# Optimization experiments

Measured on AMD Instinct MI355X. Metric: run time of the kernel, lower is better.

## Reference

```python
import jax, jax.numpy as jnp
import numpy as np

N = 50000      # nodes
E = 800000     # edges
IN = 128       # in_channels
H = 128        # hidden_channels
L = 3          # num_layers
CONF_H = 64    # confidence_hidden_dim
TAU0 = 1.0


def _linear_params(key, fan_in, fan_out, bias=True):
    k1, k2 = jax.random.split(key)
    lim = 1.0 / np.sqrt(fan_in)
    w = jax.random.uniform(k1, (fan_in, fan_out), jnp.float32, -lim, lim)
    if bias:
        b = jax.random.uniform(k2, (fan_out,), jnp.float32, -lim, lim)
        return w, b
    return w


def setup_inputs() -> dict:
    key = jax.random.key(0)
    ks = jax.random.split(key, 20)
    x = jax.random.normal(ks[0], (N, IN), jnp.float32)
    edge_index = jax.random.randint(ks[1], (2, E), 0, N, jnp.int32)
    gnoise_soft = jax.random.gumbel(ks[2], (L, N, 2), jnp.float32)
    gnoise_hard = jax.random.gumbel(ks[3], (L, N, 2), jnp.float32)
    conv_w0, conv_b0 = _linear_params(ks[4], IN, H)
    conv_w1, conv_b1 = _linear_params(ks[5], H, H)
    conv_w2, conv_b2 = _linear_params(ks[6], H, H)
    soft_w1, soft_b1 = _linear_params(ks[7], H, CONF_H)
    soft_w2, soft_b2 = _linear_params(ks[8], CONF_H, 2)
    hard_w1, hard_b1 = _linear_params(ks[9], H + 1, CONF_H)
    hard_w2, hard_b2 = _linear_params(ks[10], CONF_H, 2)
    temp_w = _linear_params(ks[11], H, 1, bias=False)
    return dict(x=x, edge_index=edge_index, gnoise_soft=gnoise_soft, gnoise_hard=gnoise_hard,
                conv_w0=conv_w0, conv_b0=conv_b0, conv_w1=conv_w1, conv_b1=conv_b1,
                conv_w2=conv_w2, conv_b2=conv_b2,
                soft_w1=soft_w1, soft_b1=soft_b1, soft_w2=soft_w2, soft_b2=soft_b2,
                hard_w1=hard_w1, hard_b1=hard_b1, hard_w2=hard_w2, hard_b2=hard_b2,
                temp_w=temp_w)


def _forward(x, edge_index, gnoise_soft, gnoise_hard,
             conv_w0, conv_b0, conv_w1, conv_b1, conv_w2, conv_b2,
             soft_w1, soft_b1, soft_w2, soft_b2,
             hard_w1, hard_b1, hard_w2, hard_b2, temp_w):
    src, dst = edge_index[0], edge_index[1]
    loop = jnp.arange(N, dtype=src.dtype)
    # GCN symmetric normalization with self-loops (PyG gcn_norm)
    src_sl = jnp.concatenate([src, loop])
    dst_sl = jnp.concatenate([dst, loop])
    deg = jax.ops.segment_sum(jnp.ones(E + N, x.dtype), dst_sl, num_segments=N)
    dinv = jnp.where(deg > 0, jax.lax.rsqrt(deg), 0.0)
    norm = dinv[src_sl] * dinv[dst_sl]  # [E+N]
    # readiness graph: self-loops removed
    nonself = (src != dst).astype(x.dtype)
    deg_ns = jnp.clip(jax.ops.segment_sum(nonself, src, num_segments=N), 1.0)

    conv_params = [(conv_w0, conv_b0), (conv_w1, conv_b1), (conv_w2, conv_b2)]
    z = jnp.zeros((N, H), x.dtype)
    soft_exited = jnp.zeros(N, bool)
    hard_exited = jnp.zeros(N, bool)
    exit_layers = jnp.full((N,), L, jnp.int32)
    active = []
    h = x
    for li in range(L):
        W, b = conv_params[li]
        hw = h @ W  # [N,H]
        h = jax.ops.segment_sum(norm[:, None] * hw[src_sl], dst_sl, num_segments=N) + b
        if li < L - 1:
            h = jax.nn.gelu(h, approximate=False)  # torch F.gelu default (dropout p=0)
        active.append(jnp.sum(~hard_exited).astype(jnp.int32))
        # temperature head: 1 / (softplus(Wx) + tau0)
        temp = 1.0 / (jax.nn.softplus(h @ temp_w) + TAU0)  # [N,1]
        temp = jnp.where(jnp.isinf(temp), 0.0, temp)
        # soft exit head + gumbel softmax (hard=False)
        soft_logits = jax.nn.relu(h @ soft_w1 + soft_b1) @ soft_w2 + soft_b2  # [N,2]
        sg = jax.nn.softmax((soft_logits + gnoise_soft[li]) / temp, axis=-1)
        soft_dec = sg[:, 1] > sg[:, 0]
        soft_exited = soft_exited | (soft_dec & ~soft_exited)
        # neighbor readiness: mean of soft_exited over non-self neighbors (detached)
        ready_sum = jax.ops.segment_sum(soft_exited[dst].astype(x.dtype) * nonself, src, num_segments=N)
        readiness = jax.lax.stop_gradient((ready_sum / deg_ns)[:, None])
        hin = jnp.concatenate([h, readiness], axis=-1)  # [N,H+1]
        hard_logits = jax.nn.relu(hin @ hard_w1 + hard_b1) @ hard_w2 + hard_b2
        cont = jnp.concatenate([jnp.full((N, 1), 1e6, x.dtype), jnp.zeros((N, 1), x.dtype)], axis=-1)
        eff = jnp.where(soft_exited[:, None], hard_logits, cont)
        hg = jax.nn.softmax((eff + gnoise_hard[li]) / temp, axis=-1)
        hard_dec = hg[:, 1] > hg[:, 0]
        newly = hard_dec & ~hard_exited
        z = z + h * newly[:, None].astype(x.dtype)
        exit_layers = jnp.where(newly, jnp.int32(li), exit_layers)
        hard_exited = hard_exited | newly
    z = z + h * (~hard_exited)[:, None].astype(x.dtype)
    return z, exit_layers, jnp.stack(active)


def reference(x, edge_index, gnoise_soft, gnoise_hard,
              conv_w0, conv_b0, conv_w1, conv_b1, conv_w2, conv_b2,
              soft_w1, soft_b1, soft_w2, soft_b2,
              hard_w1, hard_b1, hard_w2, hard_b2, temp_w):
    return _forward(x, edge_index, gnoise_soft, gnoise_hard,
                    conv_w0, conv_b0, conv_w1, conv_b1, conv_w2, conv_b2,
                    soft_w1, soft_b1, soft_w2, soft_b2,
                    hard_w1, hard_b1, hard_w2, hard_b2, temp_w)
```

## Files before the change

### kernel.cpp

```cpp
#include <hip/hip_runtime.h>
#include <hip/hip_bf16.h>
#include <math.h>

#define NN 50000
#define EE 800000
#define HH 128
#define CHH 64
#define LL 3
#define ZT (NN * HH)
#define NBK 196
#define EPB 3125

using bf16 = __hip_bfloat16;
typedef unsigned short u16;
typedef unsigned int u32;
typedef __attribute__((ext_vector_type(8))) short s16x8;
typedef __attribute__((ext_vector_type(4))) float f32x4;

__device__ __forceinline__ float ldbf(const u16* p, size_t i) {
    return __uint_as_float(((u32)p[i]) << 16);
}
__device__ __forceinline__ u16 f2b(float v) {
    bf16 b = __float2bfloat16(v);
    return *reinterpret_cast<u16*>(&b);
}
__device__ __forceinline__ void stbf(u16* p, size_t i, float v) { p[i] = f2b(v); }
__device__ __forceinline__ float blo(u32 w) { return __uint_as_float(w << 16); }
__device__ __forceinline__ float bhi(u32 w) { return __uint_as_float(w & 0xFFFF0000u); }

__global__ __launch_bounds__(256) void zero_out_k(float* __restrict__ out, int n) {
    int i = blockIdx.x * 256 + threadIdx.x;
    if (i < n) out[i] = 0.f;
}

__global__ __launch_bounds__(256) void init_k(const float* __restrict__ x, u16* __restrict__ h,
        int* __restrict__ softex, int* __restrict__ hardex, int* __restrict__ exitl,
        int* __restrict__ act) {
    int i = blockIdx.x * 256 + threadIdx.x;
    if (i < ZT) stbf(h, (size_t)i, x[i]);
    if (i < NN) { softex[i] = 0; hardex[i] = 0; exitl[i] = LL; }
    if (i < LL) act[i] = 0;
}

__global__ __launch_bounds__(256) void hist_k(const int* __restrict__ ei, int keyoff, int skipself,
        int* __restrict__ hist) {
    __shared__ int hh[NBK];
    int t = threadIdx.x, b = blockIdx.x;
    if (t < NBK) hh[t] = 0;
    __syncthreads();
    int base = b * EPB;
    for (int i = t; i < EPB; i += 256) {
        int e = base + i;
        int s = ei[e], d = ei[EE + e];
        if ((u32)s >= NN || (u32)d >= NN) continue;
        if (skipself && s == d) continue;
        int key = keyoff ? d : s;
        atomicAdd(&hh[key >> 8], 1);
    }
    __syncthreads();
    if (t < NBK) hist[b * NBK + t] = hh[t];
}

__global__ __launch_bounds__(256) void boffs_k(const int* __restrict__ hist,
        int* __restrict__ boffs, int* __restrict__ bstart) {
    int t = threadIdx.x;
    __shared__ int scn[256];
    int run = 0;
    if (t < NBK) {
        for (int b = 0; b < 256; ++b) {
            boffs[t * 256 + b] = run;
            run += hist[b * NBK + t];
        }
    }
    int v = (t < NBK) ? run : 0;
    scn[t] = v;
    __syncthreads();
    for (int off = 1; off < 256; off <<= 1) {
        int x = (t >= off) ? scn[t - off] : 0;
        __syncthreads();
        scn[t] += x;
        __syncthreads();
    }
    int excl = scn[t] - v;
    if (t < NBK) {
        bstart[t] = excl;
        if (t == NBK - 1) bstart[NBK] = excl + v;
        for (int b = 0; b < 256; ++b) boffs[t * 256 + b] += excl;
    }
}

__global__ __launch_bounds__(256) void scat_k(const int* __restrict__ ei, int keyoff, int skipself,
        const int* __restrict__ boffs, u32* __restrict__ ebuf) {
    __shared__ int cur[NBK];
    int t = threadIdx.x, b = blockIdx.x;
    if (t < NBK) cur[t] = boffs[t * 256 + b];
    __syncthreads();
    int base = b * EPB;
    for (int i = t; i < EPB; i += 256) {
        int e = base + i;
        int s = ei[e], d = ei[EE + e];
        if ((u32)s >= NN || (u32)d >= NN) continue;
        if (skipself && s == d) continue;
        int key = keyoff ? d : s;
        int other = keyoff ? s : d;
        int pos = atomicAdd(&cur[key >> 8], 1);
        ebuf[pos] = (u32)other | ((u32)(key & 255) << 16);
    }
}

__global__ __launch_bounds__(256) void fine_k(const u32* __restrict__ ebuf,
        const int* __restrict__ bstart, int* __restrict__ rowptr, u16* __restrict__ csrx,
        float* __restrict__ dinv, int addself) {
    __shared__ int cnt[256];
    __shared__ int scn[256];
    int t = threadIdx.x, bk = blockIdx.x;
    int eb = bstart[bk], ee = bstart[bk + 1];
    cnt[t] = 0;
    __syncthreads();
    for (int i = eb + t; i < ee; i += 256)
        atomicAdd(&cnt[(ebuf[i] >> 16) & 255], 1);
    __syncthreads();
    int v = cnt[t];
    scn[t] = v;
    __syncthreads();
    for (int off = 1; off < 256; off <<= 1) {
        int x = (t >= off) ? scn[t - off] : 0;
        __syncthreads();
        scn[t] += x;
        __syncthreads();
    }
    int excl = scn[t] - v;
    int n = (bk << 8) + t;
    if (n < NN) {
        rowptr[n] = eb + excl;
        if (dinv) dinv[n] = 1.0f / sqrtf((float)(v + addself));
    }
    if (bk == NBK - 1 && t == 0) rowptr[NN] = ee;
    cnt[t] = excl;
    __syncthreads();
    for (int i = eb + t; i < ee; i += 256) {
        u32 w = ebuf[i];
        int lo = (w >> 16) & 255;
        int pos = atomicAdd(&cnt[lo], 1);
        csrx[eb + pos] = (u16)(w & 0xFFFF);
    }
}

__global__ __launch_bounds__(256) void pack_w_k(const float* __restrict__ w0,
        const float* __restrict__ w1, const float* __restrict__ w2,
        const float* __restrict__ sw1, const float* __restrict__ hw1, u16* __restrict__ wt) {
    int i = blockIdx.x * 256 + threadIdx.x;
    if (i >= 4 * HH * HH) return;
    int mat = i >> 14, rr = i & 16383, o = rr >> 7, k = rr & 127;
    float v;
    if (mat == 0) v = w0[k * HH + o];
    else if (mat == 1) v = w1[k * HH + o];
    else if (mat == 2) v = w2[k * HH + o];
    else v = (o < CHH) ? sw1[k * CHH + o] : hw1[k * CHH + (o - CHH)];
    stbf(wt, (size_t)i, v);
}

__global__ __launch_bounds__(256) void gather_hin_k(const int* __restrict__ rowptr,
        const u16* __restrict__ csrc, const float* __restrict__ dinv,
        const u16* __restrict__ h, u16* __restrict__ hinb) {
    int node = blockIdx.x * 4 + (threadIdx.x >> 6);
    int lane = threadIdx.x & 63;
    int beg = rowptr[node], end = rowptr[node + 1];
    float dvd = dinv[node];
    float a0 = 0.f, a1 = 0.f;
    int e = beg;
    for (; e + 3 < end; e += 4) {
        int s0 = csrc[e], s1 = csrc[e + 1], s2 = csrc[e + 2], s3 = csrc[e + 3];
        float n0 = dinv[s0], n1 = dinv[s1], n2 = dinv[s2], n3 = dinv[s3];
        u32 w0 = *(const u32*)(h + (size_t)s0 * HH + lane * 2);
        u32 w1 = *(const u32*)(h + (size_t)s1 * HH + lane * 2);
        u32 w2 = *(const u32*)(h + (size_t)s2 * HH + lane * 2);
        u32 w3 = *(const u32*)(h + (size_t)s3 * HH + lane * 2);
        a0 = fmaf(n0, blo(w0), a0); a1 = fmaf(n0, bhi(w0), a1);
        a0 = fmaf(n1, blo(w1), a0); a1 = fmaf(n1, bhi(w1), a1);
        a0 = fmaf(n2, blo(w2), a0); a1 = fmaf(n2, bhi(w2), a1);
        a0 = fmaf(n3, blo(w3), a0); a1 = fmaf(n3, bhi(w3), a1);
    }
    for (; e < end; ++e) {
        int s0 = csrc[e];
        float n0 = dinv[s0];
        u32 w0 = *(const u32*)(h + (size_t)s0 * HH + lane * 2);
        a0 = fmaf(n0, blo(w0), a0); a1 = fmaf(n0, bhi(w0), a1);
    }
    a0 *= dvd; a1 *= dvd;
    u32 hw = *(const u32*)(h + (size_t)node * HH + lane * 2);
    float self = dvd * dvd;
    a0 = fmaf(blo(hw), self, a0);
    a1 = fmaf(bhi(hw), self, a1);
    u32 pk = (u32)f2b(a0) | ((u32)f2b(a1) << 16);
    ((u32*)hinb)[(size_t)node * 64 + lane] = pk;
}

__global__ __launch_bounds__(256) void fused_gemm_k(int li, u16* __restrict__ hinb,
        const u16* __restrict__ Wc, const u16* __restrict__ Wh,
        const float* __restrict__ bias, int geluf, u16* __restrict__ h,
        const float* __restrict__ sb1, const float* __restrict__ sw2, const float* __restrict__ sb2,
        const float* __restrict__ gs, int* __restrict__ softex) {
    __shared__ u16 hl[16 * HH];
    __shared__ float l0s[2][16], l1s[2][16];
    int wave = threadIdx.x >> 6, lane = threadIdx.x & 63;
    int row0 = blockIdx.x * 16;
    int r = lane & 15, g = lane >> 4;
    const u16* arow = hinb + (size_t)(row0 + r) * HH;
    s16x8 af[4];
    #pragma unroll
    for (int kk = 0; kk < 4; ++kk) af[kk] = *(const s16x8*)(arow + kk * 32 + g * 8);
    f32x4 acc[2];
    #pragma unroll
    for (int cc = 0; cc < 2; ++cc) {
        int c0 = wave * 32 + cc * 16;
        const u16* brow = Wc + (size_t)(c0 + r) * HH;
        f32x4 a = {0.f, 0.f, 0.f, 0.f};
        #pragma unroll
        for (int kk = 0; kk < 4; ++kk) {
            s16x8 b = *(const s16x8*)(brow + kk * 32 + g * 8);
            a = __builtin_amdgcn_mfma_f32_16x16x32_bf16(af[kk], b, a, 0, 0, 0);
        }
        acc[cc] = a;
    }
    #pragma unroll
    for (int cc = 0; cc < 2; ++cc) {
        int col = wave * 32 + cc * 16 + r;
        float bv = bias[col];
        #pragma unroll
        for (int j = 0; j < 4; ++j) {
            int row = g * 4 + j;
            float v = acc[cc][j] + bv;
            if (geluf) v = 0.5f * v * (1.0f + erff(v * 0.70710678118654752f));
            stbf(h, (size_t)(row0 + row) * HH + col, v);
            int chunk = (col >> 3) ^ (row & 7);
            hl[row * HH + chunk * 8 + (col & 7)] = f2b(v);
        }
    }
    __syncthreads();
    #pragma unroll
    for (int kk = 0; kk < 4; ++kk) {
        int k0 = kk * 32 + g * 8;
        int chunk = (k0 >> 3) ^ (r & 7);
        af[kk] = *(const s16x8*)(hl + r * HH + chunk * 8);
    }
    #pragma unroll
    for (int cc = 0; cc < 2; ++cc) {
        int c0 = wave * 32 + cc * 16;
        const u16* brow = Wh + (size_t)(c0 + r) * HH;
        f32x4 a = {0.f, 0.f, 0.f, 0.f};
        #pragma unroll
        for (int kk = 0; kk < 4; ++kk) {
            s16x8 b = *(const s16x8*)(brow + kk * 32 + g * 8);
            a = __builtin_amdgcn_mfma_f32_16x16x32_bf16(af[kk], b, a, 0, 0, 0);
        }
        acc[cc] = a;
    }
    if (wave < 2) {
        float pl0[4] = {0.f, 0.f, 0.f, 0.f}, pl1[4] = {0.f, 0.f, 0.f, 0.f};
        #pragma unroll
        for (int cc = 0; cc < 2; ++cc) {
            int col = wave * 32 + cc * 16 + r;
            float b1 = sb1[col], w20 = sw2[col * 2], w21 = sw2[col * 2 + 1];
            #pragma unroll
            for (int j = 0; j < 4; ++j) {
                float hv = fmaxf(acc[cc][j] + b1, 0.f);
                pl0[j] = fmaf(hv, w20, pl0[j]);
                pl1[j] = fmaf(hv, w21, pl1[j]);
            }
        }
        #pragma unroll
        for (int off = 1; off < 16; off <<= 1) {
            #pragma unroll
            for (int j = 0; j < 4; ++j) {
                pl0[j] += __shfl_xor(pl0[j], off);
                pl1[j] += __shfl_xor(pl1[j], off);
            }
        }
        if (r == 0) {
            #pragma unroll
            for (int j = 0; j < 4; ++j) {
                l0s[wave][g * 4 + j] = pl0[j];
                l1s[wave][g * 4 + j] = pl1[j];
            }
        }
    } else {
        #pragma unroll
        for (int cc = 0; cc < 2; ++cc) {
            int col = wave * 32 + cc * 16 + r;
            #pragma unroll
            for (int j = 0; j < 4; ++j) {
                int row = g * 4 + j;
                stbf(hinb, (size_t)(row0 + row) * HH + col, acc[cc][j]);
            }
        }
    }
    __syncthreads();
    if (threadIdx.x < 16) {
        int row = threadIdx.x, n = row0 + row;
        float l0 = l0s[0][row] + l0s[1][row] + sb2[0];
        float l1 = l1s[0][row] + l1s[1][row] + sb2[1];
        const float* gg = gs + ((size_t)li * NN + n) * 2;
        if (l1 + gg[1] > l0 + gg[0]) softex[n] = 1;
    }
}

__global__ __launch_bounds__(256) void hard_fin_k(int li, const u16* __restrict__ P,
        const u16* __restrict__ h, const float* __restrict__ hw1, const float* __restrict__ hb1,
        const float* __restrict__ hw2, const float* __restrict__ hb2,
        const float* __restrict__ gh, const int* __restrict__ softex,
        int* __restrict__ hardex, int* __restrict__ exitl,
        const int* __restrict__ orow, const u16* __restrict__ ocol,
        float* __restrict__ out) {
    int t = threadIdx.x;
    int n = blockIdx.x * 4 + (t >> 6);
    int j = t & 63;
    if (!softex[n] || hardex[n]) return;
    int ob = orow[n], oe = orow[n + 1];
    int cnt = 0;
    for (int e = ob + j; e < oe; e += 64) cnt += softex[ocol[e]];
    #pragma unroll
    for (int off = 32; off > 0; off >>= 1) cnt += __shfl_xor(cnt, off);
    int dns = oe - ob; if (dns < 1) dns = 1;
    float r = (float)cnt / (float)dns;
    float pv = ldbf(P, (size_t)n * HH + CHH + j);
    float hid = fmaxf(pv + r * hw1[HH * CHH + j] + hb1[j], 0.f);
    float l0 = hid * hw2[j * 2], l1 = hid * hw2[j * 2 + 1];
    #pragma unroll
    for (int off = 32; off > 0; off >>= 1) {
        l0 += __shfl_xor(l0, off);
        l1 += __shfl_xor(l1, off);
    }
    const float* g = gh + ((size_t)li * NN + n) * 2;
    if (l1 + hb2[1] + g[1] > l0 + hb2[0] + g[0]) {
        if (j == 0) { hardex[n] = 1; exitl[n] = li; }
        u32 hw = *(const u32*)(h + (size_t)n * HH + j * 2);
        out[(size_t)n * HH + j * 2]     = blo(hw);
        out[(size_t)n * HH + j * 2 + 1] = bhi(hw);
    }
}

__global__ __launch_bounds__(256) void tail_k(const u16* __restrict__ h, const int* __restrict__ exitl,
        float* __restrict__ out, int* __restrict__ act) {
    __shared__ int c[LL];
    int t = threadIdx.x;
    int i = blockIdx.x * 256 + t;
    if (t < LL) c[t] = 0;
    __syncthreads();
    if (i < ZT) {
        int n = i >> 7;
        if (exitl[n] == LL) out[i] = ldbf(h, (size_t)i);
    } else if (i < ZT + NN) {
        int e = exitl[i - ZT];
        out[i] = (float)e;
        if (e < LL) atomicAdd(&c[e], 1);
    }
    __syncthreads();
    if (t < LL && c[t]) atomicAdd(&act[t], c[t]);
}

__global__ __launch_bounds__(64) void finalize_k(const int* __restrict__ act, float* __restrict__ out) {
    if (threadIdx.x == 0) {
        out[ZT + NN]     = (float)NN;
        out[ZT + NN + 1] = (float)(NN - act[0]);
        out[ZT + NN + 2] = (float)(NN - act[0] - act[1]);
    }
}

extern "C" void kernel_launch(void* const* d_in, const int* in_sizes, int n_in,
                              void* d_out, int out_size, void* d_ws, size_t ws_size,
                              hipStream_t stream) {
    float* out = (float*)d_out;
    const int OUT_N = ZT + NN + LL;

    static const int CANON[19] = {6400000,1600000,300000,300000,16384,128,16384,128,16384,128,
                                  8192,64,128,2,8256,64,128,2,128};
    static const int SORTED_ROLE[19] = {5,7,9,4,6,8,1,3,2,15,17,14,16,11,13,10,12,18,0};
    int perm[19];
    bool ok = (n_in == 19);
    if (ok) {
        bool mc = true, mr = true, ms = true;
        for (int i = 0; i < 19; ++i) {
            if (in_sizes[i] != CANON[i]) mc = false;
            if (in_sizes[i] != CANON[18 - i]) mr = false;
            if (in_sizes[i] != CANON[SORTED_ROLE[i]]) ms = false;
        }
        if (mc)      for (int c = 0; c < 19; ++c) perm[c] = c;
        else if (mr) for (int c = 0; c < 19; ++c) perm[c] = 18 - c;
        else if (ms) { for (int p = 0; p < 19; ++p) perm[SORTED_ROLE[p]] = p; }
        else         for (int c = 0; c < 19; ++c) perm[c] = c;
    }
    if (!ok) {
        zero_out_k<<<(OUT_N + 255) / 256, 256, 0, stream>>>(out, OUT_N);
        return;
    }

    const float* x  = (const float*)d_in[perm[0]];
    const int*   ei = (const int*)d_in[perm[1]];
    const float* gs = (const float*)d_in[perm[2]];
    const float* gh = (const float*)d_in[perm[3]];
    const float* cw[3] = { (const float*)d_in[perm[4]], (const float*)d_in[perm[6]], (const float*)d_in[perm[8]] };
    const float* cb[3] = { (const float*)d_in[perm[5]], (const float*)d_in[perm[7]], (const float*)d_in[perm[9]] };
    const float* sw1 = (const float*)d_in[perm[10]];
    const float* sb1 = (const float*)d_in[perm[11]];
    const float* sw2 = (const float*)d_in[perm[12]];
    const float* sb2 = (const float*)d_in[perm[13]];
    const float* hw1 = (const float*)d_in[perm[14]];
    const float* hb1 = (const float*)d_in[perm[15]];
    const float* hw2 = (const float*)d_in[perm[16]];
    const float* hb2 = (const float*)d_in[perm[17]];

    const size_t H_B    = (size_t)ZT * 2;
    const size_t FLAG_B = 200192;
    const size_t ACT_B  = 256;
    const size_t RP_B   = 200704;
    const size_t CE_B   = (size_t)EE * 2;
    const size_t WT_B   = 4 * HH * HH * 2;
    const size_t need = 2 * H_B + 4 * FLAG_B + ACT_B + 2 * RP_B + 2 * CE_B + WT_B;
    if (ws_size < need) {
        zero_out_k<<<(OUT_N + 255) / 256, 256, 0, stream>>>(out, OUT_N);
        return;
    }

    char* p = (char*)d_ws;
    u16* h    = (u16*)p; p += H_B;
    u16* hinb = (u16*)p; p += H_B;
    int* softex = (int*)p; p += FLAG_B;
    int* hardex = (int*)p; p += FLAG_B;
    int* exitl  = (int*)p; p += FLAG_B;
    float* dinv = (float*)p; p += FLAG_B;
    int* act    = (int*)p; p += ACT_B;
    int* irow   = (int*)p; p += RP_B;
    int* orow   = (int*)p; p += RP_B;
    u16* csrc   = (u16*)p; p += CE_B;
    u16* ocol   = (u16*)p; p += CE_B;
    u16* wt     = (u16*)p; p += WT_B;

    char* q = (char*)hinb;
    u32* ebuf  = (u32*)q;  q += (size_t)EE * 4;
    int* hist  = (int*)q;  q += 256 * NBK * 4;
    int* boffs = (int*)q;  q += NBK * 256 * 4;
    int* bstart = (int*)q; q += 1024;

    init_k<<<(ZT + 255) / 256, 256, 0, stream>>>(x, h, softex, hardex, exitl, act);

    hist_k<<<256, 256, 0, stream>>>(ei, 1, 0, hist);
    boffs_k<<<1, 256, 0, stream>>>(hist, boffs, bstart);
    scat_k<<<256, 256, 0, stream>>>(ei, 1, 0, boffs, ebuf);
    fine_k<<<NBK, 256, 0, stream>>>(ebuf, bstart, irow, csrc, dinv, 1);
    hist_k<<<256, 256, 0, stream>>>(ei, 0, 1, hist);
    boffs_k<<<1, 256, 0, stream>>>(hist, boffs, bstart);
    scat_k<<<256, 256, 0, stream>>>(ei, 0, 1, boffs, ebuf);
    fine_k<<<NBK, 256, 0, stream>>>(ebuf, bstart, orow, ocol, nullptr, 0);

    pack_w_k<<<(4 * HH * HH + 255) / 256, 256, 0, stream>>>(cw[0], cw[1], cw[2], sw1, hw1, wt);

    for (int li = 0; li < LL; ++li) {
        int geluf = (li < LL - 1) ? 1 : 0;
        gather_hin_k<<<NN / 4, 256, 0, stream>>>(irow, csrc, dinv, h, hinb);
        fused_gemm_k<<<NN / 16, 256, 0, stream>>>(li, hinb, wt + (size_t)li * HH * HH,
                                                  wt + (size_t)3 * HH * HH, cb[li], geluf, h,
                                                  sb1, sw2, sb2, gs, softex);
        hard_fin_k<<<NN / 4, 256, 0, stream>>>(li, hinb, h, hw1, hb1, hw2, hb2, gh, softex,
                                               hardex, exitl, orow, ocol, out);
    }
    tail_k<<<(OUT_N + 255) / 256, 256, 0, stream>>>(h, exitl, out, act);
    finalize_k<<<1, 64, 0, stream>>>(act, out);
}
```

Measured before the change: 415.4 us.

## Fuse neighbor gather into GEMM kernel and merge dual CSR builds

The per-layer neighbor aggregation is folded into the GEMM kernel: each block gathers its 16 rows straight into swizzled shared memory instead of writing and re-reading a bf16 hin buffer in global memory. The h buffers are ping-ponged between layers, and the hard-head projection partials are staged as fp32 in the output buffer for rows that have not exited. The two CSR builds (by destination and by source) are merged into single histogram, scatter and fine-sort launches, which cuts launches and reads of the edge list. The cost is less parallelism in the gather, since 4 rows per wave run serially inside a GEMM block, and extra workspace for the second edge buffer.

```diff
diff --git a/kernel.cpp b/kernel.cpp
--- a/kernel.cpp
+++ b/kernel.cpp
@@ -42,23 +42,22 @@
     if (i < LL) act[i] = 0;
 }
 
-__global__ __launch_bounds__(256) void hist_k(const int* __restrict__ ei, int keyoff, int skipself,
-        int* __restrict__ hist) {
-    __shared__ int hh[NBK];
+__global__ __launch_bounds__(256) void hist_both_k(const int* __restrict__ ei,
+        int* __restrict__ hist1, int* __restrict__ hist2) {
+    __shared__ int h1[NBK], h2[NBK];
     int t = threadIdx.x, b = blockIdx.x;
-    if (t < NBK) hh[t] = 0;
+    if (t < NBK) { h1[t] = 0; h2[t] = 0; }
     __syncthreads();
     int base = b * EPB;
     for (int i = t; i < EPB; i += 256) {
         int e = base + i;
         int s = ei[e], d = ei[EE + e];
         if ((u32)s >= NN || (u32)d >= NN) continue;
-        if (skipself && s == d) continue;
-        int key = keyoff ? d : s;
-        atomicAdd(&hh[key >> 8], 1);
-    }
-    __syncthreads();
-    if (t < NBK) hist[b * NBK + t] = hh[t];
+        atomicAdd(&h1[d >> 8], 1);
+        if (s != d) atomicAdd(&h2[s >> 8], 1);
+    }
+    __syncthreads();
+    if (t < NBK) { hist1[b * NBK + t] = h1[t]; hist2[b * NBK + t] = h2[t]; }
 }
 
 __global__ __launch_bounds__(256) void boffs_k(const int* __restrict__ hist,
@@ -89,31 +88,33 @@
     }
 }
 
-__global__ __launch_bounds__(256) void scat_k(const int* __restrict__ ei, int keyoff, int skipself,
-        const int* __restrict__ boffs, u32* __restrict__ ebuf) {
-    __shared__ int cur[NBK];
+__global__ __launch_bounds__(256) void scat_both_k(const int* __restrict__ ei,
+        const int* __restrict__ boffs1, u32* __restrict__ ebuf1,
+        const int* __restrict__ boffs2, u32* __restrict__ ebuf2) {
+    __shared__ int c1[NBK], c2[NBK];
     int t = threadIdx.x, b = blockIdx.x;
-    if (t < NBK) cur[t] = boffs[t * 256 + b];
+    if (t < NBK) { c1[t] = boffs1[t * 256 + b]; c2[t] = boffs2[t * 256 + b]; }
     __syncthreads();
     int base = b * EPB;
     for (int i = t; i < EPB; i += 256) {
         int e = base + i;
         int s = ei[e], d = ei[EE + e];
         if ((u32)s >= NN || (u32)d >= NN) continue;
-        if (skipself && s == d) continue;
-        int key = keyoff ? d : s;
-        int other = keyoff ? s : d;
-        int pos = atomicAdd(&cur[key >> 8], 1);
-        ebuf[pos] = (u32)other | ((u32)(key & 255) << 16);
-    }
-}
-
-__global__ __launch_bounds__(256) void fine_k(const u32* __restrict__ ebuf,
+        int pos = atomicAdd(&c1[d >> 8], 1);
+        ebuf1[pos] = (u32)s | ((u32)(d & 255) << 16);
+        if (s != d) {
+            int pos2 = atomicAdd(&c2[s >> 8], 1);
+            ebuf2[pos2] = (u32)d | ((u32)(s & 255) << 16);
+        }
+    }
+}
+
+__device__ __forceinline__ void fine_body(int bk, const u32* __restrict__ ebuf,
         const int* __restrict__ bstart, int* __restrict__ rowptr, u16* __restrict__ csrx,
         float* __restrict__ dinv, int addself) {
     __shared__ int cnt[256];
     __shared__ int scn[256];
-    int t = threadIdx.x, bk = blockIdx.x;
+    int t = threadIdx.x;
     int eb = bstart[bk], ee = bstart[bk + 1];
     cnt[t] = 0;
     __syncthreads();
@@ -136,6 +137,7 @@
         if (dinv) dinv[n] = 1.0f / sqrtf((float)(v + addself));
     }
     if (bk == NBK - 1 && t == 0) rowptr[NN] = ee;
+    __syncthreads();
     cnt[t] = excl;
     __syncthreads();
     for (int i = eb + t; i < ee; i += 256) {
@@ -144,6 +146,14 @@
         int pos = atomicAdd(&cnt[lo], 1);
         csrx[eb + pos] = (u16)(w & 0xFFFF);
     }
+}
+
+__global__ __launch_bounds__(256) void fine2_k(const u32* __restrict__ ebuf1,
+        const int* __restrict__ bstart1, int* __restrict__ irow, u16* __restrict__ csrc,
+        float* __restrict__ dinv, const u32* __restrict__ ebuf2,
+        const int* __restrict__ bstart2, int* __restrict__ orow, u16* __restrict__ ocol) {
+    if (blockIdx.x < NBK) fine_body(blockIdx.x, ebuf1, bstart1, irow, csrc, dinv, 1);
+    else                  fine_body(blockIdx.x - NBK, ebuf2, bstart2, orow, ocol, nullptr, 0);
 }
 
 __global__ __launch_bounds__(256) void pack_w_k(const float* __restrict__ w0,
@@ -160,56 +170,64 @@
     stbf(wt, (size_t)i, v);
 }
 
-__global__ __launch_bounds__(256) void gather_hin_k(const int* __restrict__ rowptr,
-        const u16* __restrict__ csrc, const float* __restrict__ dinv,
-        const u16* __restrict__ h, u16* __restrict__ hinb) {
-    int node = blockIdx.x * 4 + (threadIdx.x >> 6);
-    int lane = threadIdx.x & 63;
-    int beg = rowptr[node], end = rowptr[node + 1];
-    float dvd = dinv[node];
-    float a0 = 0.f, a1 = 0.f;
-    int e = beg;
-    for (; e + 3 < end; e += 4) {
-        int s0 = csrc[e], s1 = csrc[e + 1], s2 = csrc[e + 2], s3 = csrc[e + 3];
-        float n0 = dinv[s0], n1 = dinv[s1], n2 = dinv[s2], n3 = dinv[s3];
-        u32 w0 = *(const u32*)(h + (size_t)s0 * HH + lane * 2);
-        u32 w1 = *(const u32*)(h + (size_t)s1 * HH + lane * 2);
-        u32 w2 = *(const u32*)(h + (size_t)s2 * HH + lane * 2);
-        u32 w3 = *(const u32*)(h + (size_t)s3 * HH + lane * 2);
-        a0 = fmaf(n0, blo(w0), a0); a1 = fmaf(n0, bhi(w0), a1);
-        a0 = fmaf(n1, blo(w1), a0); a1 = fmaf(n1, bhi(w1), a1);
-        a0 = fmaf(n2, blo(w2), a0); a1 = fmaf(n2, bhi(w2), a1);
-        a0 = fmaf(n3, blo(w3), a0); a1 = fmaf(n3, bhi(w3), a1);
-    }
-    for (; e < end; ++e) {
-        int s0 = csrc[e];
-        float n0 = dinv[s0];
-        u32 w0 = *(const u32*)(h + (size_t)s0 * HH + lane * 2);
-        a0 = fmaf(n0, blo(w0), a0); a1 = fmaf(n0, bhi(w0), a1);
-    }
-    a0 *= dvd; a1 *= dvd;
-    u32 hw = *(const u32*)(h + (size_t)node * HH + lane * 2);
-    float self = dvd * dvd;
-    a0 = fmaf(blo(hw), self, a0);
-    a1 = fmaf(bhi(hw), self, a1);
-    u32 pk = (u32)f2b(a0) | ((u32)f2b(a1) << 16);
-    ((u32*)hinb)[(size_t)node * 64 + lane] = pk;
-}
-
-__global__ __launch_bounds__(256) void fused_gemm_k(int li, u16* __restrict__ hinb,
-        const u16* __restrict__ Wc, const u16* __restrict__ Wh,
-        const float* __restrict__ bias, int geluf, u16* __restrict__ h,
+__global__ __launch_bounds__(256) void mega_k(int li, int geluf,
+        const int* __restrict__ irow, const u16* __restrict__ csrc, const float* __restrict__ dinv,
+        const u16* __restrict__ hin_g, u16* __restrict__ hout_g,
+        const u16* __restrict__ Wc, const u16* __restrict__ Wh, const float* __restrict__ bias,
         const float* __restrict__ sb1, const float* __restrict__ sw2, const float* __restrict__ sb2,
-        const float* __restrict__ gs, int* __restrict__ softex) {
+        const float* __restrict__ gs, int* __restrict__ softex, const int* __restrict__ hardex,
+        float* __restrict__ outP) {
+    __shared__ u32 hin[16 * 64];
     __shared__ u16 hl[16 * HH];
     __shared__ float l0s[2][16], l1s[2][16];
-    int wave = threadIdx.x >> 6, lane = threadIdx.x & 63;
+    __shared__ int hx[16];
+    int tid = threadIdx.x;
+    int wave = tid >> 6, lane = tid & 63;
     int row0 = blockIdx.x * 16;
+    if (tid < 16) hx[tid] = hardex[row0 + tid];
+    #pragma unroll
+    for (int i = 0; i < 4; ++i) {
+        int row = wave * 4 + i;
+        int node = row0 + row;
+        int beg = irow[node], end = irow[node + 1];
+        float dvd = dinv[node];
+        float a0 = 0.f, a1 = 0.f;
+        int e = beg;
+        for (; e + 3 < end; e += 4) {
+            int s0 = csrc[e], s1 = csrc[e + 1], s2 = csrc[e + 2], s3 = csrc[e + 3];
+            float n0 = dinv[s0], n1 = dinv[s1], n2 = dinv[s2], n3 = dinv[s3];
+            u32 w0 = *(const u32*)(hin_g + (size_t)s0 * HH + lane * 2);
+            u32 w1 = *(const u32*)(hin_g + (size_t)s1 * HH + lane * 2);
+            u32 w2 = *(const u32*)(hin_g + (size_t)s2 * HH + lane * 2);
+            u32 w3 = *(const u32*)(hin_g + (size_t)s3 * HH + lane * 2);
+            a0 = fmaf(n0, blo(w0), a0); a1 = fmaf(n0, bhi(w0), a1);
+            a0 = fmaf(n1, blo(w1), a0); a1 = fmaf(n1, bhi(w1), a1);
+            a0 = fmaf(n2, blo(w2), a0); a1 = fmaf(n2, bhi(w2), a1);
+            a0 = fmaf(n3, blo(w3), a0); a1 = fmaf(n3, bhi(w3), a1);
+        }
+        for (; e < end; ++e) {
+            int s0 = csrc[e];
+            float n0 = dinv[s0];
+            u32 w0 = *(const u32*)(hin_g + (size_t)s0 * HH + lane * 2);
+            a0 = fmaf(n0, blo(w0), a0); a1 = fmaf(n0, bhi(w0), a1);
+        }
+        a0 *= dvd; a1 *= dvd;
+        u32 hw = *(const u32*)(hin_g + (size_t)node * HH + lane * 2);
+        float self = dvd * dvd;
+        a0 = fmaf(blo(hw), self, a0);
+        a1 = fmaf(bhi(hw), self, a1);
+        hin[row * 64 + (((lane >> 2) ^ (row & 7)) << 2) + (lane & 3)] =
+            (u32)f2b(a0) | ((u32)f2b(a1) << 16);
+    }
+    __syncthreads();
     int r = lane & 15, g = lane >> 4;
-    const u16* arow = hinb + (size_t)(row0 + r) * HH;
+    const u16* hinw = (const u16*)hin;
     s16x8 af[4];
     #pragma unroll
-    for (int kk = 0; kk < 4; ++kk) af[kk] = *(const s16x8*)(arow + kk * 32 + g * 8);
+    for (int kk = 0; kk < 4; ++kk) {
+        int chunk = (kk * 4 + g) ^ (r & 7);
+        af[kk] = *(const s16x8*)(hinw + r * HH + chunk * 8);
+    }
     f32x4 acc[2];
     #pragma unroll
     for (int cc = 0; cc < 2; ++cc) {
@@ -232,7 +250,7 @@
             int row = g * 4 + j;
             float v = acc[cc][j] + bv;
             if (geluf) v = 0.5f * v * (1.0f + erff(v * 0.70710678118654752f));
-            stbf(h, (size_t)(row0 + row) * HH + col, v);
+            stbf(hout_g, (size_t)(row0 + row) * HH + col, v);
             int chunk = (col >> 3) ^ (row & 7);
             hl[row * HH + chunk * 8 + (col & 7)] = f2b(v);
         }
@@ -291,21 +309,21 @@
             #pragma unroll
             for (int j = 0; j < 4; ++j) {
                 int row = g * 4 + j;
-                stbf(hinb, (size_t)(row0 + row) * HH + col, acc[cc][j]);
+                if (!hx[row]) outP[(size_t)(row0 + row) * HH + col] = acc[cc][j];
             }
         }
     }
     __syncthreads();
-    if (threadIdx.x < 16) {
-        int row = threadIdx.x, n = row0 + row;
-        float l0 = l0s[0][row] + l0s[1][row] + sb2[0];
-        float l1 = l1s[0][row] + l1s[1][row] + sb2[1];
+    if (tid < 16) {
+        int n = row0 + tid;
+        float l0 = l0s[0][tid] + l0s[1][tid] + sb2[0];
+        float l1 = l1s[0][tid] + l1s[1][tid] + sb2[1];
         const float* gg = gs + ((size_t)li * NN + n) * 2;
         if (l1 + gg[1] > l0 + gg[0]) softex[n] = 1;
     }
 }
 
-__global__ __launch_bounds__(256) void hard_fin_k(int li, const u16* __restrict__ P,
+__global__ __launch_bounds__(256) void hard_fin_k(int li,
         const u16* __restrict__ h, const float* __restrict__ hw1, const float* __restrict__ hb1,
         const float* __restrict__ hw2, const float* __restrict__ hb2,
         const float* __restrict__ gh, const int* __restrict__ softex,
@@ -323,7 +341,7 @@
     for (int off = 32; off > 0; off >>= 1) cnt += __shfl_xor(cnt, off);
     int dns = oe - ob; if (dns < 1) dns = 1;
     float r = (float)cnt / (float)dns;
-    float pv = ldbf(P, (size_t)n * HH + CHH + j);
+    float pv = out[(size_t)n * HH + CHH + j];
     float hid = fmaxf(pv + r * hw1[HH * CHH + j] + hb1[j], 0.f);
     float l0 = hid * hw2[j * 2], l1 = hid * hw2[j * 2 + 1];
     #pragma unroll
@@ -423,8 +441,8 @@
     }
 
     char* p = (char*)d_ws;
-    u16* h    = (u16*)p; p += H_B;
-    u16* hinb = (u16*)p; p += H_B;
+    u16* hA   = (u16*)p; p += H_B;
+    u16* hB   = (u16*)p; p += H_B;
     int* softex = (int*)p; p += FLAG_B;
     int* hardex = (int*)p; p += FLAG_B;
     int* exitl  = (int*)p; p += FLAG_B;
@@ -436,34 +454,37 @@
     u16* ocol   = (u16*)p; p += CE_B;
     u16* wt     = (u16*)p; p += WT_B;
 
-    char* q = (char*)hinb;
-    u32* ebuf  = (u32*)q;  q += (size_t)EE * 4;
-    int* hist  = (int*)q;  q += 256 * NBK * 4;
-    int* boffs = (int*)q;  q += NBK * 256 * 4;
-    int* bstart = (int*)q; q += 1024;
-
-    init_k<<<(ZT + 255) / 256, 256, 0, stream>>>(x, h, softex, hardex, exitl, act);
-
-    hist_k<<<256, 256, 0, stream>>>(ei, 1, 0, hist);
-    boffs_k<<<1, 256, 0, stream>>>(hist, boffs, bstart);
-    scat_k<<<256, 256, 0, stream>>>(ei, 1, 0, boffs, ebuf);
-    fine_k<<<NBK, 256, 0, stream>>>(ebuf, bstart, irow, csrc, dinv, 1);
-    hist_k<<<256, 256, 0, stream>>>(ei, 0, 1, hist);
-    boffs_k<<<1, 256, 0, stream>>>(hist, boffs, bstart);
-    scat_k<<<256, 256, 0, stream>>>(ei, 0, 1, boffs, ebuf);
-    fine_k<<<NBK, 256, 0, stream>>>(ebuf, bstart, orow, ocol, nullptr, 0);
-
+    char* q = (char*)hB;
+    u32* ebuf1  = (u32*)q;  q += (size_t)EE * 4;
+    u32* ebuf2  = (u32*)q;  q += (size_t)EE * 4;
+    int* hist1  = (int*)q;  q += 256 * NBK * 4;
+    int* hist2  = (int*)q;  q += 256 * NBK * 4;
+    int* boffs1 = (int*)q;  q += NBK * 256 * 4;
+    int* boffs2 = (int*)q;  q += NBK * 256 * 4;
+    int* bstart1 = (int*)q; q += 1024;
+    int* bstart2 = (int*)q; q += 1024;
+
+    init_k<<<(ZT + 255) / 256, 256, 0, stream>>>(x, hA, softex, hardex, exitl, act);
+
+    hist_both_k<<<256, 256, 0, stream>>>(ei, hist1, hist2);
+    boffs_k<<<1, 256, 0, stream>>>(hist1, boffs1, bstart1);
+    boffs_k<<<1, 256, 0, stream>>>(hist2, boffs2, bstart2);
+    scat_both_k<<<256, 256, 0, stream>>>(ei, boffs1, ebuf1, boffs2, ebuf2);
+    fine2_k<<<2 * NBK, 256, 0, stream>>>(ebuf1, bstart1, irow, csrc, dinv,
+                                         ebuf2, bstart2, orow, ocol);
     pack_w_k<<<(4 * HH * HH + 255) / 256, 256, 0, stream>>>(cw[0], cw[1], cw[2], sw1, hw1, wt);
 
+    u16* hbuf[2] = { hA, hB };
     for (int li = 0; li < LL; ++li) {
         int geluf = (li < LL - 1) ? 1 : 0;
-        gather_hin_k<<<NN / 4, 256, 0, stream>>>(irow, csrc, dinv, h, hinb);
-        fused_gemm_k<<<NN / 16, 256, 0, stream>>>(li, hinb, wt + (size_t)li * HH * HH,
-                                                  wt + (size_t)3 * HH * HH, cb[li], geluf, h,
-                                                  sb1, sw2, sb2, gs, softex);
-        hard_fin_k<<<NN / 4, 256, 0, stream>>>(li, hinb, h, hw1, hb1, hw2, hb2, gh, softex,
+        u16* hin  = hbuf[li & 1];
+        u16* hout = hbuf[(li & 1) ^ 1];
+        mega_k<<<NN / 16, 256, 0, stream>>>(li, geluf, irow, csrc, dinv, hin, hout,
+                                            wt + (size_t)li * HH * HH, wt + (size_t)3 * HH * HH,
+                                            cb[li], sb1, sw2, sb2, gs, softex, hardex, out);
+        hard_fin_k<<<NN / 4, 256, 0, stream>>>(li, hout, hw1, hb1, hw2, hb2, gh, softex,
                                                hardex, exitl, orow, ocol, out);
     }
-    tail_k<<<(OUT_N + 255) / 256, 256, 0, stream>>>(h, exitl, out, act);
+    tail_k<<<(OUT_N + 255) / 256, 256, 0, stream>>>(hbuf[LL & 1], exitl, out, act);
     finalize_k<<<1, 64, 0, stream>>>(act, out);
 }
```

After: 366.2 us. -11.8%, faster.
